# Kernel optimization log

Measured on AMD Instinct MI355X. Metric: run time of the kernel, lower is better.

The kernel has to match this reference:

```python
import jax, jax.numpy as jnp
import numpy as np

STRIDES = (128, 64, 32, 16, 8)
FM_SHAPES = ((6, 10), (12, 20), (24, 40), (48, 80), (96, 160))
RATIOS = np.array([1.0, 2.0, 3.0])
BASE_SIZE = 4
POS_THR, NEG_THR, IGNORE = 0.5, 0.4, -1.0
ALPHA, GAMMA, SIGMA = 0.25, 2.0, 3.0


def _cell_anchors(stride):
    # classic generate_anchors: base 4x4 anchor, 3 aspect ratios, scale=stride
    w = h = float(BASE_SIZE)
    ctr = (BASE_SIZE - 1) / 2.0
    size = w * h
    ws = np.round(np.sqrt(size / RATIOS))
    hs = np.round(ws * RATIOS)
    a = np.stack([ctr - 0.5 * (ws - 1), ctr - 0.5 * (hs - 1),
                  ctr + 0.5 * (ws - 1), ctr + 0.5 * (hs - 1)], 1)
    aw = a[:, 2] - a[:, 0] + 1
    ah = a[:, 3] - a[:, 1] + 1
    cx = a[:, 0] + 0.5 * (aw - 1)
    cy = a[:, 1] + 0.5 * (ah - 1)
    sw = aw * stride
    sh = ah * stride
    return np.stack([cx - 0.5 * (sw - 1), cy - 0.5 * (sh - 1),
                     cx + 0.5 * (sw - 1), cy + 0.5 * (sh - 1)], 1)


def _all_anchors():
    outs = []
    for (h, w), s in zip(FM_SHAPES, STRIDES):
        cell = _cell_anchors(s)  # [3,4]
        sx = np.tile((np.arange(w) * s)[None, :], (h, 1)).reshape(-1)
        sy = np.tile((np.arange(h) * s)[:, None], (1, w)).reshape(-1)
        shifts = np.stack([sx, sy, sx, sy], 1)  # [h*w,4]
        outs.append((cell[None] + shifts[:, None]).reshape(-1, 4))
    return np.concatenate(outs, 0).astype(np.float32)  # [A,4]


def box_overlap(b, g):
    ab = (b[:, 2] - b[:, 0] + 1) * (b[:, 3] - b[:, 1] + 1)
    ag = (g[:, 2] - g[:, 0] + 1) * (g[:, 3] - g[:, 1] + 1)
    iw = jnp.clip(jnp.minimum(b[:, None, 2], g[None, :, 2]) - jnp.maximum(b[:, None, 0], g[None, :, 0]) + 1, 0)
    ih = jnp.clip(jnp.minimum(b[:, None, 3], g[None, :, 3]) - jnp.maximum(b[:, None, 1], g[None, :, 1]) + 1, 0)
    inter = iw * ih
    return inter / (ab[:, None] + ag[None, :] - inter)


def bbox_transform_inv(anc, dlt):
    w = anc[..., 2] - anc[..., 0] + 1
    h = anc[..., 3] - anc[..., 1] + 1
    cx = anc[..., 0] + 0.5 * (w - 1)
    cy = anc[..., 1] + 0.5 * (h - 1)
    mx = jnp.log(jnp.asarray(1000.0 / 16, dlt.dtype))
    pw = jnp.exp(jnp.minimum(dlt[..., 2], mx)) * w
    ph = jnp.exp(jnp.minimum(dlt[..., 3], mx)) * h
    pcx = dlt[..., 0] * w + cx
    pcy = dlt[..., 1] * h + cy
    return jnp.stack([pcx - 0.5 * (pw - 1), pcy - 0.5 * (ph - 1),
                      pcx + 0.5 * (pw - 1), pcy + 0.5 * (ph - 1)], -1)


def bbox_transform(anc, gt):
    aw = anc[..., 2] - anc[..., 0] + 1
    ah = anc[..., 3] - anc[..., 1] + 1
    acx = anc[..., 0] + 0.5 * (aw - 1)
    acy = anc[..., 1] + 0.5 * (ah - 1)
    gw = gt[..., 2] - gt[..., 0] + 1
    gh = gt[..., 3] - gt[..., 1] + 1
    gcx = gt[..., 0] + 0.5 * (gw - 1)
    gcy = gt[..., 1] + 0.5 * (gh - 1)
    return jnp.stack([(gcx - acx) / aw, (gcy - acy) / ah,
                      jnp.log(gw / aw), jnp.log(gh / ah)], -1)


def conv3x3(x, w, b):
    y = jax.lax.conv_general_dilated(x, w, (1, 1), 'SAME',
                                     dimension_numbers=('NCHW', 'OIHW', 'NCHW'))
    return y + b[None, :, None, None]


def _head(feat, cls_w, cls_b, box_w, box_b, score_w, score_b,
          bpred_w, bpred_b, iou_w, iou_b, num_w, num_b):
    n = feat.shape[0]
    c = feat
    for i in range(4):
        c = jax.nn.relu(conv3x3(c, cls_w[i], cls_b[i]))
    cls_prob = jax.nn.sigmoid(conv3x3(c, score_w, score_b))
    num_prob = conv3x3(c, num_w, num_b)
    r = feat
    for i in range(4):
        r = jax.nn.relu(conv3x3(r, box_w[i], box_b[i]))
    offsets = conv3x3(r, bpred_w, bpred_b)
    iou_prob = conv3x3(r, iou_w, iou_b)
    rs = lambda t, ch: t.transpose(0, 2, 3, 1).reshape(n, -1, ch)
    return rs(cls_prob, 2), rs(num_prob, 2), rs(offsets, 8), rs(iou_prob, 2)


def _forward(feats, gt_boxes, im_info, cls_w, cls_b, box_w, box_b,
             score_w, score_b, bpred_w, bpred_b, iou_w, iou_b, num_w, num_b):
    outs = [_head(f, cls_w, cls_b, box_w, box_b, score_w, score_b,
                  bpred_w, bpred_b, iou_w, iou_b, num_w, num_b) for f in feats]
    cls_prob = jnp.concatenate([o[0] for o in outs], 1)  # [n,A,2]
    num_prob = jnp.concatenate([o[1] for o in outs], 1)  # [n,A,2]
    offsets = jnp.concatenate([o[2] for o in outs], 1)   # [n,A,8]
    iou_prob = jnp.concatenate([o[3] for o in outs], 1)  # [n,A,2]
    anchors = jnp.asarray(_all_anchors())                # [A,4]
    A = anchors.shape[0]
    n = cls_prob.shape[0]
    G = gt_boxes.shape[1]
    counts = im_info[:, 5]
    gidx = jnp.arange(G, dtype=jnp.float32)

    def anchor_target_one(gt, cnt):
        valid = (gidx < cnt) & (gt[:, 4] != IGNORE)
        ov = jnp.where(valid[None, :], box_overlap(anchors, gt[:, :4]), -1.0)
        top2, idx = jax.lax.top_k(ov, 2)  # [A,2]
        labels = jnp.where(top2 >= POS_THR, 1.0,
                           jnp.where(top2 < NEG_THR, 0.0, -1.0))
        tgt = bbox_transform(anchors[:, None, :], gt[idx, :4])  # [A,2,4]
        return labels, tgt.reshape(-1, 4)

    rpn_labels, target_boxes = jax.vmap(anchor_target_one)(gt_boxes, counts)
    rpn_labels = jax.lax.stop_gradient(rpn_labels)        # [n,A,2]
    target_boxes = jax.lax.stop_gradient(target_boxes)    # [n,2A,4]
    anchors2 = jnp.repeat(anchors, 2, axis=0)             # [2A,4] interleaved

    def iou_target_one(gt, cnt, off):
        dt = bbox_transform_inv(anchors2, off.reshape(-1, 4))  # [2A,4]
        keep = ((gidx < cnt) & (gt[:, 4] != IGNORE)).astype(dt.dtype)
        ov = box_overlap(dt, gt[:, :4]) * keep[None, :]        # [2A,G]
        ov = ov.reshape(A, 2, G)
        a, b = ov[:, 0], ov[:, 1]
        i1 = jnp.argmax(a, 1)
        av = jnp.take_along_axis(a, i1[:, None], 1)
        b = b.at[jnp.arange(A), i1].set(0.0)
        bv = jnp.max(b, 1, keepdims=True)
        return jnp.concatenate([av, bv], 1)                    # [A,2]

    ious_target = jax.lax.stop_gradient(
        jax.vmap(iou_target_one)(gt_boxes, counts, offsets))

    a, b = rpn_labels[..., 0], rpn_labels[..., 1]
    ignores = b - (a == 0).astype(b.dtype) * (b != 0).astype(b.dtype)
    labels = jnp.stack([a, ignores], 2).reshape(n, -1)     # [n,2A]

    # focal (sigmoid_cross_entropy_retina)
    p = cls_prob.reshape(n, -1, 1)                          # [n,2A,1]
    mask = (labels != IGNORE).astype(p.dtype)
    onehot = ((labels * mask) == 1).astype(p.dtype)[..., None]
    pos = (1 - p) ** GAMMA * onehot * jnp.log(p)
    neg = p ** GAMMA * (1 - onehot) * jnp.log(1 - p)
    npos = jnp.maximum((labels > 0).astype(p.dtype).sum(), 1.0)
    cls_loss = (-(ALPHA * pos + (1 - ALPHA) * neg).sum(-1) * mask).sum() / npos

    # smooth_l1_loss_retina (sigma=3)
    off4 = offsets.reshape(n, -1, 4)                        # [n,2A,4]
    diff = off4 - target_boxes
    ad = jnp.abs(diff)
    s2 = SIGMA * SIGMA
    sl1 = jnp.where(ad < 1.0 / s2, 0.5 * s2 * diff * diff, ad - 0.5 / s2)
    posm = (labels > 0).astype(off4.dtype)
    bbox_loss = (sl1.sum(-1) * posm).sum() / jnp.maximum(posm.sum(), 1.0)

    # iou_l1_loss
    lab2 = labels.reshape(n, -1, 2)                         # [n,A,2]
    ioumask = (lab2 > 0).astype(iou_prob.dtype)
    iou_loss = (jnp.abs(iou_prob.reshape(n, -1, 2) - ious_target) * ioumask).sum() \
        / jnp.maximum(ioumask.sum(), 1.0)

    # softmax_loss over num-per-anchor predictions
    nlabels = (lab2 > 0).sum(2).reshape(-1) - 1             # [n*A] in {-1,0,1}
    score = num_prob.reshape(-1, 2)
    logp = jax.nn.log_softmax(score, -1)
    nm = (nlabels != -1)
    vl = jnp.where(nm, nlabels, 0)
    nmf = nm.astype(score.dtype)
    num_loss = (-(jnp.take_along_axis(logp, vl[:, None], 1)[:, 0]) * nmf).sum() \
        / jnp.maximum(nmf.sum(), 1.0)

    return jnp.stack([cls_loss, 2.0 * bbox_loss, 2.0 * iou_loss, num_loss])


def setup_inputs() -> dict:
    key = jax.random.key(0)
    ks = jax.random.split(key, 24)
    n, G = 2, 32
    inp = {}
    for i, (h, w) in enumerate(FM_SHAPES):
        inp[f"feat_p{7 - i}"] = jax.random.normal(ks[i], (n, 256, h, w), jnp.float32) * 0.5
    x1 = jax.random.uniform(ks[5], (n, G), minval=0.0, maxval=900.0)
    y1 = jax.random.uniform(ks[6], (n, G), minval=0.0, maxval=500.0)
    bw = jax.random.uniform(ks[7], (n, G), minval=32.0, maxval=300.0)
    bh = jax.random.uniform(ks[8], (n, G), minval=32.0, maxval=300.0)
    inp["gt_boxes"] = jnp.stack([x1, y1, x1 + bw, y1 + bh, jnp.ones((n, G))], -1).astype(jnp.float32)
    inp["im_info"] = jnp.tile(jnp.array([[768., 1280., 1., 768., 1280., 24.]], jnp.float32), (n, 1))
    std = 0.01
    inp["cls_w"] = jax.random.normal(ks[9], (4, 256, 256, 3, 3), jnp.float32) * std
    inp["cls_b"] = jnp.zeros((4, 256), jnp.float32)
    inp["box_w"] = jax.random.normal(ks[10], (4, 256, 256, 3, 3), jnp.float32) * std
    inp["box_b"] = jnp.zeros((4, 256), jnp.float32)
    prior_bias = -float(np.log((1 - 0.01) / 0.01))
    inp["score_w"] = jax.random.normal(ks[11], (6, 256, 3, 3), jnp.float32) * std
    inp["score_b"] = jnp.full((6,), prior_bias, jnp.float32)
    inp["bpred_w"] = jax.random.normal(ks[12], (24, 256, 3, 3), jnp.float32) * std
    inp["bpred_b"] = jnp.zeros((24,), jnp.float32)
    inp["iou_w"] = jax.random.normal(ks[13], (6, 256, 3, 3), jnp.float32) * std
    inp["iou_b"] = jnp.zeros((6,), jnp.float32)
    inp["num_w"] = jax.random.normal(ks[14], (6, 256, 3, 3), jnp.float32) * std
    inp["num_b"] = jnp.zeros((6,), jnp.float32)
    return inp


def reference(feat_p7, feat_p6, feat_p5, feat_p4, feat_p3, gt_boxes, im_info,
              cls_w, cls_b, box_w, box_b, score_w, score_b, bpred_w, bpred_b,
              iou_w, iou_b, num_w, num_b):
    feats = [feat_p7, feat_p6, feat_p5, feat_p4, feat_p3]
    return _forward(feats, gt_boxes, im_info, cls_w, cls_b, box_w, box_b,
                    score_w, score_b, bpred_w, bpred_b, iou_w, iou_b, num_w, num_b)
```

## Files before the change

kernel.cpp:

```cpp
#include <hip/hip_runtime.h>
#include <math.h>

#define A_TOTAL 61380
#define NGT 32
#define PTOT 21472

typedef _Float16 f16;
typedef f16 f16x8 __attribute__((ext_vector_type(8)));
typedef float f32x4 __attribute__((ext_vector_type(4)));

__device__ __constant__ int LV_H[5]    = {6, 12, 24, 48, 96};
__device__ __constant__ int LV_W[5]    = {10, 20, 40, 80, 160};
__device__ __constant__ int LV_PB[5]   = {0, 96, 404, 1496, 5596};
__device__ __constant__ int LV_TX[5]   = {1, 2, 3, 5, 10};

typedef __attribute__((address_space(1))) const void* gptr_t;
typedef __attribute__((address_space(3))) void* lptr_t;
__device__ __forceinline__ void cp16_g2l(const void* g, void* l) {
  __builtin_amdgcn_global_load_lds((gptr_t)g, (lptr_t)l, 16, 0, 0);
}

__device__ __forceinline__ void get_tile8(int t, int& lv, int& y0, int& x0)
{
  int local;
  if (t >= 44)      { lv = 4; local = t - 44; }
  else if (t >= 14) { lv = 3; local = t - 14; }
  else if (t >= 5)  { lv = 2; local = t - 5; }
  else if (t >= 1)  { lv = 1; local = t - 1; }
  else              { lv = 0; local = 0; }
  int tX = LV_TX[lv];
  y0 = (local / tX) * 8;
  x0 = (local % tX) * 16;
}

__device__ __forceinline__ void get_tile16(int t, int& lv, int& y0, int& x0)
{
  int local;
  if (t >= 24)      { lv = 4; local = t - 24; }
  else if (t >= 9)  { lv = 3; local = t - 9; }
  else if (t >= 3)  { lv = 2; local = t - 3; }
  else if (t >= 1)  { lv = 1; local = t - 1; }
  else              { lv = 0; local = 0; }
  int tX = LV_TX[lv];
  y0 = (local / tX) * 16;
  x0 = (local % tX) * 16;
}

__device__ __forceinline__ int padded_off(int p)
{
  if (p >= 5100)      { int po = p - 5100; int y = po / 160, x = po - y * 160; return 5596 + (y + 1) * 162 + x + 1; }
  else if (p >= 1260) { int po = p - 1260; int y = po / 80,  x = po - y * 80;  return 1496 + (y + 1) * 82  + x + 1; }
  else if (p >= 300)  { int po = p - 300;  int y = po / 40,  x = po - y * 40;  return 404  + (y + 1) * 42  + x + 1; }
  else if (p >= 60)   { int po = p - 60;   int y = po / 20,  x = po - y * 20;  return 96   + (y + 1) * 22  + x + 1; }
  else                { int y = p / 10, x = p - y * 10;                         return (y + 1) * 12 + x + 1; }
}

__global__ __launch_bounds__(64) void zero_borders(f16* __restrict__ act)
{
  int e = blockIdx.x, b = blockIdx.y, z = blockIdx.z;
  int lv, e0;
  if (e >= 496)      { lv = 4; e0 = e - 496; }
  else if (e >= 236) { lv = 3; e0 = e - 236; }
  else if (e >= 104) { lv = 2; e0 = e - 104; }
  else if (e >= 36)  { lv = 1; e0 = e - 36; }
  else               { lv = 0; e0 = e; }
  int Hp = LV_H[lv] + 2, Wp = LV_W[lv] + 2;
  int y, x;
  if (e0 < Wp)          { y = 0;      x = e0; }
  else if (e0 < 2 * Wp) { y = Hp - 1; x = e0 - Wp; }
  else { int e2 = e0 - 2 * Wp; y = 1 + (e2 >> 1); x = (e2 & 1) ? (Wp - 1) : 0; }
  f16* dst = act + ((size_t)z * 2 * PTOT + (size_t)b * PTOT + LV_PB[lv] + y * Wp + x) * 256
           + threadIdx.x * 4;
  *(uint2*)dst = (uint2){0u, 0u};
}

__global__ __launch_bounds__(256) void feats_to_nhwc(
    const float* __restrict__ f0, const float* __restrict__ f1,
    const float* __restrict__ f2, const float* __restrict__ f3,
    const float* __restrict__ f4, f16* __restrict__ act)
{
  const int b = blockIdx.z;
  const int c0 = blockIdx.y * 32;
  const int p0 = blockIdx.x * 32;
  const int tx = threadIdx.x & 31, ty = threadIdx.x >> 5;
  __shared__ float tl[32][33];

  int p = p0 + tx;
  const float* src = f0; int po = 0;
  if (p >= 5100)      { src = f4; po = p - 5100; }
  else if (p >= 1260) { src = f3; po = p - 1260; }
  else if (p >= 300)  { src = f2; po = p - 300;  }
  else if (p >= 60)   { src = f1; po = p - 60;   }
  else                { src = f0; po = p;        }
  int HW = (p >= 5100) ? 15360 : (p >= 1260) ? 3840 : (p >= 300) ? 960 : (p >= 60) ? 240 : 60;

#pragma unroll
  for (int k = 0; k < 4; ++k) {
    int c = c0 + ty + k * 8;
    float v = 0.f;
    if (p < 20460) v = src[((size_t)b * 256 + c) * HW + po];
    tl[ty + k * 8][tx] = v;
  }
  __syncthreads();
#pragma unroll
  for (int k = 0; k < 4; ++k) {
    int pp = p0 + ty + k * 8;
    if (pp < 20460)
      act[((size_t)b * PTOT + padded_off(pp)) * 256 + c0 + tx] = (f16)tl[tx][ty + k * 8];
  }
}

__global__ __launch_bounds__(256) void prep_tower_w3(
    const float* __restrict__ cls_w, const float* __restrict__ box_w,
    f16* __restrict__ wT)
{
  int blk = blockIdx.x;
  int l = blk >> 8, co = blk & 255;
  const float* src = (l < 4 ? cls_w + (size_t)l * 589824
                            : box_w + (size_t)(l - 4) * 589824)
                   + (size_t)co * 2304;
  __shared__ f16 sm[2304];
  int t = threadIdx.x;
#pragma unroll
  for (int j = 0; j < 9; ++j) sm[t + j * 256] = (f16)src[t + j * 256];
  __syncthreads();
#pragma unroll
  for (int it = 0; it < 2; ++it) {
    int c = t + it * 256;
    if (c < 288) {
      int tap = c >> 5, s = c & 31;
      f16x8 v;
#pragma unroll
      for (int e = 0; e < 8; ++e) v[e] = sm[(s * 8 + e) * 9 + tap];
      *(f16x8*)(wT + ((((size_t)l * 9 + tap) * 32 + s) * 256 + co) * 8) = v;
    }
  }
}

__global__ void prep_head_w3(const float* __restrict__ sw, const float* __restrict__ nw,
                             const float* __restrict__ bw, const float* __restrict__ iw,
                             const float* __restrict__ sb, const float* __restrict__ nb2,
                             const float* __restrict__ bb, const float* __restrict__ ib,
                             f16* __restrict__ wH, float* __restrict__ hb)
{
  int idx = blockIdx.x * 256 + threadIdx.x;
  if (idx < 18432) {
    int p = idx / 9216, rem = idx - p * 9216;
    int tap = rem / 1024, rem2 = rem - tap * 1024;
    int s = rem2 >> 5, co = rem2 & 31;
    int C1 = p ? 24 : 6;
    const float* w1 = p ? bw : sw;
    const float* w2 = p ? iw : nw;
    f16x8 v;
#pragma unroll
    for (int e = 0; e < 8; ++e) {
      int ci = s * 8 + e;
      float x = 0.f;
      if (co < C1)          x = w1[((size_t)co * 256 + ci) * 9 + tap];
      else if (co < C1 + 6) x = w2[((size_t)(co - C1) * 256 + ci) * 9 + tap];
      v[e] = (f16)x;
    }
    *(f16x8*)(wH + (size_t)idx * 8) = v;
  }
  if (idx < 64) {
    int pp = idx >> 5, jj = idx & 31;
    int C1b = pp ? 24 : 6;
    const float* b1 = pp ? bb : sb;
    const float* b2 = pp ? ib : nb2;
    float bv = 0.f;
    if (jj < C1b)          bv = b1[jj];
    else if (jj < C1b + 6) bv = b2[jj - C1b];
    hb[idx] = bv;
  }
}

__global__ __launch_bounds__(256, 2) void conv_mfma_tower4(
    const f16* __restrict__ in_cls, f16* __restrict__ out_cls,
    const f16* __restrict__ in_box, f16* __restrict__ out_box,
    const f16* __restrict__ wT, const float* __restrict__ cls_b,
    const float* __restrict__ box_b, int layer)
{
  int lv, y0, x0;
  get_tile8(blockIdx.x, lv, y0, x0);
  const int H = LV_H[lv], W = LV_W[lv], Wp = W + 2, pbase = LV_PB[lv];
  const int b = blockIdx.y;
  const int z = blockIdx.z, tw = z >> 1, cog = z & 1;
  const f16* in  = tw ? in_box : in_cls;
  f16*       out = tw ? out_box : out_cls;
  const f16* wB = wT + (size_t)(tw * 4 + layer) * 2304 * 256;
  const float* bias = (tw ? box_b : cls_b) + layer * 256;

  const int tid = threadIdx.x;
  const int lane = tid & 63, wid = tid >> 6;
  const int m = lane & 15, q = lane >> 4;
  const int mrow = (wid & 1) * 4;
  const int ncol = (wid >> 1) * 64;

  __shared__ __align__(16) f16 Bs[4096 * 8];

  f32x4 acc[4][4];
#pragma unroll
  for (int i = 0; i < 4; ++i)
#pragma unroll
    for (int j = 0; j < 4; ++j) acc[i][j] = (f32x4){0.f, 0.f, 0.f, 0.f};

  const f16* inb = in + (size_t)(b * PTOT + pbase) * 256;
  const f16* pA = inb + ((size_t)(y0 + mrow) * Wp + x0 + m) * 256 + q * 8;

  for (int cb = 0; cb < 8; ++cb) {
    __syncthreads();
#pragma unroll
    for (int it = 0; it < 16; ++it) {
      int u = tid + it * 256;
      int tap = u >> 9, r = u & 511;
      int s = r >> 7, c = r & 127;
      cp16_g2l(wB + (((size_t)(tap * 32 + cb * 4 + s)) * 256 + cog * 128 + c) * 8,
               Bs + (size_t)u * 8);
    }
    __syncthreads();
    const f16* pAc = pA + cb * 32;
#pragma unroll
    for (int tap = 0; tap < 9; ++tap) {
      const int ky = tap / 3, kx = tap - ky * 3;
      f16x8 af[4], bf[4];
#pragma unroll
      for (int mb = 0; mb < 4; ++mb)
        af[mb] = *(const f16x8*)(pAc + ((size_t)(mb + ky) * Wp + kx) * 256);
      if (tap < 8) {
#pragma unroll
        for (int nb = 0; nb < 4; ++nb)
          bf[nb] = *(const f16x8*)(Bs + (size_t)(tap * 512 + q * 128 + ncol + nb * 16 + m) * 8);
      } else {
#pragma unroll
        for (int nb = 0; nb < 4; ++nb)
          bf[nb] = *(const f16x8*)(wB + (((size_t)(256 + cb * 4 + q)) * 256 + cog * 128 + ncol + nb * 16 + m) * 8);
      }
#pragma unroll
      for (int mb = 0; mb < 4; ++mb)
#pragma unroll
        for (int nb = 0; nb < 4; ++nb)
          acc[mb][nb] = __builtin_amdgcn_mfma_f32_16x16x32_f16(af[mb], bf[nb], acc[mb][nb], 0, 0, 0);
    }
  }

  f16* outb = out + (size_t)(b * PTOT + pbase) * 256;
#pragma unroll
  for (int mb = 0; mb < 4; ++mb) {
    int y = y0 + mrow + mb;
    if (y >= H) continue;
#pragma unroll
    for (int nb = 0; nb < 4; ++nb) {
      int co = cog * 128 + ncol + nb * 16 + m;
      float bi = bias[co];
#pragma unroll
      for (int r = 0; r < 4; ++r) {
        int x = x0 + q * 4 + r;
        if (x < W) {
          float v = fmaxf(acc[mb][nb][r] + bi, 0.f);
          outb[((size_t)(y + 1) * Wp + x + 1) * 256 + co] = (f16)v;
        }
      }
    }
  }
}

__global__ __launch_bounds__(256) void conv_mfma_head3(
    const f16* __restrict__ in_cls, const f16* __restrict__ in_box,
    const f16* __restrict__ wH, const float* __restrict__ hb,
    float* __restrict__ cls_prob, float* __restrict__ num_prob,
    float* __restrict__ offsets, float* __restrict__ iou_prob)
{
  int lv, y0, x0;
  get_tile16(blockIdx.x, lv, y0, x0);
  const int H = LV_H[lv], W = LV_W[lv], Wp = W + 2, pbase = LV_PB[lv];
  const int b = blockIdx.y, z = blockIdx.z;
  const f16* in = z ? in_box : in_cls;
  const f16* wB = wH + (size_t)z * 2304 * 32;
  const float* hbz = hb + z * 32;
  float* o1 = z ? offsets : cls_prob;
  float* o2 = z ? iou_prob : num_prob;
  const int C1 = z ? 24 : 6, P1 = z ? 8 : 2, SIG = z ? 0 : 1;

  const int tid = threadIdx.x;
  const int lane = tid & 63, wid = tid >> 6;
  const int m = lane & 15, q = lane >> 4;

  f32x4 acc[4][2];
#pragma unroll
  for (int i = 0; i < 4; ++i) { acc[i][0] = (f32x4){0,0,0,0}; acc[i][1] = (f32x4){0,0,0,0}; }

  const f16* inb = in + (size_t)(b * PTOT + pbase) * 256;
  const f16* pA = inb + ((size_t)(y0 + wid * 4) * Wp + x0 + m) * 256 + q * 8;
  const f16* pB = wB + ((size_t)q * 32 + m) * 8;

  for (int cb = 0; cb < 8; ++cb) {
    const f16* pAc = pA + cb * 32;
    const f16* pBc = pB + (size_t)cb * 4 * 32 * 8;
#pragma unroll
    for (int tap = 0; tap < 9; ++tap) {
      const int ky = tap / 3, kx = tap - ky * 3;
      f16x8 af[4], bf[2];
#pragma unroll
      for (int mb = 0; mb < 4; ++mb)
        af[mb] = *(const f16x8*)(pAc + ((size_t)(mb + ky) * Wp + kx) * 256);
#pragma unroll
      for (int nb = 0; nb < 2; ++nb)
        bf[nb] = *(const f16x8*)(pBc + (size_t)tap * 8192 + nb * 128);
#pragma unroll
      for (int mb = 0; mb < 4; ++mb)
#pragma unroll
        for (int nb = 0; nb < 2; ++nb)
          acc[mb][nb] = __builtin_amdgcn_mfma_f32_16x16x32_f16(af[mb], bf[nb], acc[mb][nb], 0, 0, 0);
    }
  }

  const int robase = (lv == 0 ? 0 : lv == 1 ? 60 : lv == 2 ? 300 : lv == 3 ? 1260 : 5100) * 3;
#pragma unroll
  for (int mb = 0; mb < 4; ++mb) {
    int y = y0 + wid * 4 + mb;
    if (y >= H) continue;
#pragma unroll
    for (int nb = 0; nb < 2; ++nb) {
      int j = nb * 16 + m;
      if (j >= C1 + 6) continue;
      float bi = hbz[j];
#pragma unroll
      for (int r = 0; r < 4; ++r) {
        int x = x0 + q * 4 + r;
        if (x < W) {
          float v = acc[mb][nb][r] + bi;
          int row0 = robase + (y * W + x) * 3;
          if (j < C1) {
            if (SIG) v = 1.f / (1.f + expf(-v));
            int jd = j / P1;
            o1[((size_t)b * A_TOTAL + row0 + jd) * P1 + (j - jd * P1)] = v;
          } else {
            int jj = j - C1;
            o2[((size_t)b * A_TOTAL + row0 + (jj >> 1)) * 2 + (jj & 1)] = v;
          }
        }
      }
    }
  }
}

__global__ void gen_anchors(float* __restrict__ anchors, float* __restrict__ accum)
{
  int i = blockIdx.x * 256 + threadIdx.x;
  if (blockIdx.x == 0 && threadIdx.x < 8) accum[threadIdx.x] = 0.f;
  if (i >= A_TOTAL) return;
  int off, s, Wl;
  if (i >= 15300)     { off = 15300; s = 8;   Wl = 160; }
  else if (i >= 3780) { off = 3780;  s = 16;  Wl = 80;  }
  else if (i >= 900)  { off = 900;   s = 32;  Wl = 40;  }
  else if (i >= 180)  { off = 180;   s = 64;  Wl = 20;  }
  else                { off = 0;     s = 128; Wl = 10;  }
  int r = i - off;
  int cell = r / 3, a = r - cell * 3;
  int y = cell / Wl, x = cell - y * Wl;
  float wsv = (a == 0) ? 4.f : (a == 1) ? 3.f : 2.f;
  float hsv = (a == 0) ? 4.f : 6.f;
  float sw = wsv * (float)s, sh = hsv * (float)s;
  float cx = (float)(x * s) + 1.5f, cy = (float)(y * s) + 1.5f;
  anchors[i * 4 + 0] = cx - 0.5f * (sw - 1.f);
  anchors[i * 4 + 1] = cy - 0.5f * (sh - 1.f);
  anchors[i * 4 + 2] = cx + 0.5f * (sw - 1.f);
  anchors[i * 4 + 3] = cy + 0.5f * (sh - 1.f);
}

__global__ __launch_bounds__(256) void anchor_target(
    const float* __restrict__ anchors, const float* __restrict__ gt,
    const float* __restrict__ iminfo, float* __restrict__ rpn, float* __restrict__ tgt)
{
  int i = blockIdx.x * 256 + threadIdx.x;
  int b = blockIdx.y;
  if (i >= A_TOTAL) return;
  float cnt = iminfo[b * 6 + 5];
  float ax1 = anchors[i*4+0], ay1 = anchors[i*4+1], ax2 = anchors[i*4+2], ay2 = anchors[i*4+3];
  float aw = ax2 - ax1 + 1.f, ah = ay2 - ay1 + 1.f, ab = aw * ah;
  float v1 = -1e30f, v2 = -1e30f; int i1 = 0, i2 = 0;
  for (int g = 0; g < NGT; ++g) {
    const float* gp = gt + (b * NGT + g) * 5;
    float ov = -1.f;
    if ((float)g < cnt && gp[4] != -1.f) {
      float iw = fmaxf(fminf(ax2, gp[2]) - fmaxf(ax1, gp[0]) + 1.f, 0.f);
      float ih = fmaxf(fminf(ay2, gp[3]) - fmaxf(ay1, gp[1]) + 1.f, 0.f);
      float inter = iw * ih;
      float ag = (gp[2] - gp[0] + 1.f) * (gp[3] - gp[1] + 1.f);
      ov = inter / (ab + ag - inter);
    }
    if (ov > v1)      { v2 = v1; i2 = i1; v1 = ov; i1 = g; }
    else if (ov > v2) { v2 = ov; i2 = g; }
  }
  float l1 = (v1 >= 0.5f) ? 1.f : ((v1 < 0.4f) ? 0.f : -1.f);
  float l2 = (v2 >= 0.5f) ? 1.f : ((v2 < 0.4f) ? 0.f : -1.f);
  rpn[(b * A_TOTAL + i) * 2 + 0] = l1;
  rpn[(b * A_TOTAL + i) * 2 + 1] = l2;
  float acx = ax1 + 0.5f * (aw - 1.f), acy = ay1 + 0.5f * (ah - 1.f);
  int idx2[2] = {i1, i2};
#pragma unroll
  for (int k = 0; k < 2; ++k) {
    const float* gp = gt + (b * NGT + idx2[k]) * 5;
    float gw = gp[2] - gp[0] + 1.f, gh = gp[3] - gp[1] + 1.f;
    float gcx = gp[0] + 0.5f * (gw - 1.f), gcy = gp[1] + 0.5f * (gh - 1.f);
    float* o = tgt + ((size_t)(b * 2 * A_TOTAL) + i * 2 + k) * 4;
    o[0] = (gcx - acx) / aw;  o[1] = (gcy - acy) / ah;
    o[2] = logf(gw / aw);     o[3] = logf(gh / ah);
  }
}

__global__ __launch_bounds__(256) void iou_target(
    const float* __restrict__ anchors, const float* __restrict__ gt,
    const float* __restrict__ iminfo, const float* __restrict__ offsets,
    float* __restrict__ ioust)
{
  int i = blockIdx.x * 256 + threadIdx.x;
  int b = blockIdx.y;
  if (i >= A_TOTAL) return;
  float cnt = iminfo[b * 6 + 5];
  float ax1 = anchors[i*4+0], ay1 = anchors[i*4+1], ax2 = anchors[i*4+2], ay2 = anchors[i*4+3];
  float aw = ax2 - ax1 + 1.f, ah = ay2 - ay1 + 1.f;
  float acx = ax1 + 0.5f * (aw - 1.f), acy = ay1 + 0.5f * (ah - 1.f);
  const float mx = 4.135166556742356f;
  float bx[2][4];
#pragma unroll
  for (int k = 0; k < 2; ++k) {
    const float* d = offsets + ((size_t)(b * A_TOTAL) + i) * 8 + k * 4;
    float pw = expf(fminf(d[2], mx)) * aw;
    float ph = expf(fminf(d[3], mx)) * ah;
    float pcx = d[0] * aw + acx, pcy = d[1] * ah + acy;
    bx[k][0] = pcx - 0.5f * (pw - 1.f); bx[k][1] = pcy - 0.5f * (ph - 1.f);
    bx[k][2] = pcx + 0.5f * (pw - 1.f); bx[k][3] = pcy + 0.5f * (ph - 1.f);
  }
  float area0 = (bx[0][2]-bx[0][0]+1.f) * (bx[0][3]-bx[0][1]+1.f);
  float area1 = (bx[1][2]-bx[1][0]+1.f) * (bx[1][3]-bx[1][1]+1.f);
  float av = -1e30f; int i1 = 0;
  for (int g = 0; g < NGT; ++g) {
    const float* gp = gt + (b * NGT + g) * 5;
    float keep = ((float)g < cnt && gp[4] != -1.f) ? 1.f : 0.f;
    float ag = (gp[2] - gp[0] + 1.f) * (gp[3] - gp[1] + 1.f);
    float iw = fmaxf(fminf(bx[0][2], gp[2]) - fmaxf(bx[0][0], gp[0]) + 1.f, 0.f);
    float ih = fmaxf(fminf(bx[0][3], gp[3]) - fmaxf(bx[0][1], gp[1]) + 1.f, 0.f);
    float inter = iw * ih;
    float ov = inter / (area0 + ag - inter) * keep;
    if (ov > av) { av = ov; i1 = g; }
  }
  float bv = -1e30f;
  for (int g = 0; g < NGT; ++g) {
    float val = 0.f;
    if (g != i1) {
      const float* gp = gt + (b * NGT + g) * 5;
      float keep = ((float)g < cnt && gp[4] != -1.f) ? 1.f : 0.f;
      float ag = (gp[2] - gp[0] + 1.f) * (gp[3] - gp[1] + 1.f);
      float iw = fmaxf(fminf(bx[1][2], gp[2]) - fmaxf(bx[1][0], gp[0]) + 1.f, 0.f);
      float ih = fmaxf(fminf(bx[1][3], gp[3]) - fmaxf(bx[1][1], gp[1]) + 1.f, 0.f);
      float inter = iw * ih;
      val = inter / (area1 + ag - inter) * keep;
    }
    bv = fmaxf(bv, val);
  }
  ioust[(b * A_TOTAL + i) * 2 + 0] = av;
  ioust[(b * A_TOTAL + i) * 2 + 1] = bv;
}

__global__ __launch_bounds__(256) void loss_reduce(
    const float* __restrict__ cls_prob, const float* __restrict__ num_prob,
    const float* __restrict__ offsets,  const float* __restrict__ iou_prob,
    const float* __restrict__ rpn,      const float* __restrict__ tgt,
    const float* __restrict__ ioust,    float* __restrict__ accum)
{
  int i = blockIdx.x * 256 + threadIdx.x;
  int b = blockIdx.y;
  float cls_s = 0.f, npos = 0.f, bb_s = 0.f, iou_s = 0.f, num_s = 0.f, num_c = 0.f;
  float la = 0.f, ign = 0.f;
  if (i < A_TOTAL) {
    int base = b * A_TOTAL + i;
    la = rpn[base * 2 + 0];
    float lb = rpn[base * 2 + 1];
    ign = lb - ((la == 0.f && lb != 0.f) ? 1.f : 0.f);
    float lab2[2] = {la, ign};
#pragma unroll
    for (int j = 0; j < 2; ++j) {
      float l = lab2[j];
      float mask = (l != -1.f) ? 1.f : 0.f;
      bool oh = (l * mask) == 1.f;
      float p = cls_prob[base * 2 + j];
      float term = oh ? (0.25f * (1.f - p) * (1.f - p) * logf(p))
                      : (0.75f * p * p * logf(1.f - p));
      cls_s += -term * mask;
      if (l > 0.f) {
        npos += 1.f;
#pragma unroll
        for (int c = 0; c < 4; ++c) {
          float d = offsets[(size_t)base * 8 + j * 4 + c]
                  - tgt[((size_t)(b * 2 * A_TOTAL) + i * 2 + j) * 4 + c];
          float ad = fabsf(d);
          bb_s += (ad < 1.f / 9.f) ? (4.5f * d * d) : (ad - 0.5f / 9.f);
        }
        iou_s += fabsf(iou_prob[base * 2 + j] - ioust[base * 2 + j]);
      }
    }
    int nl = ((la > 0.f) ? 1 : 0) + ((ign > 0.f) ? 1 : 0) - 1;
    if (nl != -1) {
      float s0 = num_prob[base * 2], s1 = num_prob[base * 2 + 1];
      float mm = fmaxf(s0, s1);
      float lse = mm + logf(expf(s0 - mm) + expf(s1 - mm));
      num_s += lse - ((nl == 0) ? s0 : s1);
      num_c += 1.f;
    }
  }
  __shared__ float red[6][4];
  float vals[6] = {cls_s, npos, bb_s, iou_s, num_s, num_c};
  int lane = threadIdx.x & 63, wid = threadIdx.x >> 6;
#pragma unroll
  for (int qq = 0; qq < 6; ++qq) {
    float v = vals[qq];
#pragma unroll
    for (int o = 32; o > 0; o >>= 1) v += __shfl_down(v, o);
    if (lane == 0) red[qq][wid] = v;
  }
  __syncthreads();
  if (threadIdx.x < 6) {
    float s = red[threadIdx.x][0] + red[threadIdx.x][1] + red[threadIdx.x][2] + red[threadIdx.x][3];
    atomicAdd(&accum[threadIdx.x], s);
  }
}

__global__ void finalize_loss(const float* __restrict__ acc, float* __restrict__ out)
{
  float npos = fmaxf(acc[1], 1.f);
  out[0] = acc[0] / npos;
  out[1] = 2.f * acc[2] / npos;
  out[2] = 2.f * acc[3] / npos;
  out[3] = acc[4] / fmaxf(acc[5], 1.f);
}

extern "C" void kernel_launch(void* const* d_in, const int* in_sizes, int n_in,
                              void* d_out, int out_size, void* d_ws, size_t ws_size,
                              hipStream_t stream)
{
  (void)in_sizes; (void)n_in; (void)out_size; (void)ws_size;
  const float* feat[5];
  for (int i = 0; i < 5; ++i) feat[i] = (const float*)d_in[i];
  const float* gt      = (const float*)d_in[5];
  const float* iminfo  = (const float*)d_in[6];
  const float* cls_w   = (const float*)d_in[7];
  const float* cls_b   = (const float*)d_in[8];
  const float* box_w   = (const float*)d_in[9];
  const float* box_b   = (const float*)d_in[10];
  const float* score_w = (const float*)d_in[11];
  const float* score_b = (const float*)d_in[12];
  const float* bpred_w = (const float*)d_in[13];
  const float* bpred_b = (const float*)d_in[14];
  const float* iou_w   = (const float*)d_in[15];
  const float* iou_b   = (const float*)d_in[16];
  const float* num_w   = (const float*)d_in[17];
  const float* num_b   = (const float*)d_in[18];

  const size_t ACT2 = (size_t)2 * PTOT * 256;
  f16* actF = (f16*)d_ws;
  f16* actA = actF + ACT2;
  f16* actB = actA + ACT2;
  f16* actC = actB + ACT2;
  f16* wT   = actC + ACT2;
  f16* wH   = wT + (size_t)8 * 2304 * 256;
  float* hb = (float*)(wH + (size_t)2 * 2304 * 32);

  float* cls_prob = (float*)actA;
  float* num_prob = cls_prob + 2 * A_TOTAL * 2;
  float* offsets  = num_prob + 2 * A_TOTAL * 2;
  float* iou_prob = offsets + 2 * A_TOTAL * 8;
  float* anchors  = iou_prob + 2 * A_TOTAL * 2;
  float* rpn      = anchors + A_TOTAL * 4;
  float* tgt      = rpn + 2 * A_TOTAL * 2;
  float* ioust    = tgt + 2 * 2 * A_TOTAL * 4;
  float* accum    = ioust + 2 * A_TOTAL * 2;

  prep_tower_w3<<<dim3(2048), 256, 0, stream>>>(cls_w, box_w, wT);
  prep_head_w3<<<dim3(72), 256, 0, stream>>>(
      score_w, num_w, bpred_w, iou_w, score_b, num_b, bpred_b, iou_b, wH, hb);
  zero_borders<<<dim3(1012, 2, 4), 64, 0, stream>>>(actF);
  feats_to_nhwc<<<dim3(640, 8, 2), 256, 0, stream>>>(
      feat[0], feat[1], feat[2], feat[3], feat[4], actF);

  dim3 tg(164, 2, 4);
  conv_mfma_tower4<<<tg, 256, 0, stream>>>(actF, actA, actF, actC, wT, cls_b, box_b, 0);
  conv_mfma_tower4<<<tg, 256, 0, stream>>>(actA, actB, actC, actF, wT, cls_b, box_b, 1);
  conv_mfma_tower4<<<tg, 256, 0, stream>>>(actB, actA, actF, actC, wT, cls_b, box_b, 2);
  conv_mfma_tower4<<<tg, 256, 0, stream>>>(actA, actB, actC, actF, wT, cls_b, box_b, 3);

  conv_mfma_head3<<<dim3(84, 2, 2), 256, 0, stream>>>(
      actB, actF, wH, hb, cls_prob, num_prob, offsets, iou_prob);

  dim3 agrid((A_TOTAL + 255) / 256, 2);
  gen_anchors<<<dim3((A_TOTAL + 255) / 256), 256, 0, stream>>>(anchors, accum);
  anchor_target<<<agrid, 256, 0, stream>>>(anchors, gt, iminfo, rpn, tgt);
  iou_target<<<agrid, 256, 0, stream>>>(anchors, gt, iminfo, offsets, ioust);
  loss_reduce<<<agrid, 256, 0, stream>>>(cls_prob, num_prob, offsets, iou_prob,
                                         rpn, tgt, ioust, accum);
  finalize_loss<<<1, 1, 0, stream>>>(accum, (float*)d_out);
}
```

Baseline: 902.2 us.

## Stage input halo tile in LDS and reuse rows across kernel taps

The tower conv kernel now copies the 10x18-pixel input halo for each 32-channel block into shared memory, where it used to read activations straight from global memory once per tap. Rows are loaded once per kx and reused across the three ky taps. The weight staging buffer shrinks to six taps, with the last-row taps read from global memory. This is meant to cut redundant global activation reads, at the cost of fewer weights staged in LDS and more global weight loads.

```diff
diff --git a/kernel.cpp b/kernel.cpp
--- a/kernel.cpp
+++ b/kernel.cpp
@@ -174,7 +174,7 @@
   }
 }
 
-__global__ __launch_bounds__(256, 2) void conv_mfma_tower4(
+__global__ __launch_bounds__(256, 2) void conv_mfma_tower5(
     const f16* __restrict__ in_cls, f16* __restrict__ out_cls,
     const f16* __restrict__ in_box, f16* __restrict__ out_box,
     const f16* __restrict__ wT, const float* __restrict__ cls_b,
@@ -196,7 +196,8 @@
   const int mrow = (wid & 1) * 4;
   const int ncol = (wid >> 1) * 64;
 
-  __shared__ __align__(16) f16 Bs[4096 * 8];
+  __shared__ __align__(16) f16 Al[720 * 8];
+  __shared__ __align__(16) f16 Bl[3072 * 8];
 
   f32x4 acc[4][4];
 #pragma unroll
@@ -205,41 +206,54 @@
     for (int j = 0; j < 4; ++j) acc[i][j] = (f32x4){0.f, 0.f, 0.f, 0.f};
 
   const f16* inb = in + (size_t)(b * PTOT + pbase) * 256;
-  const f16* pA = inb + ((size_t)(y0 + mrow) * Wp + x0 + m) * 256 + q * 8;
 
   for (int cb = 0; cb < 8; ++cb) {
     __syncthreads();
 #pragma unroll
-    for (int it = 0; it < 16; ++it) {
+    for (int it = 0; it < 3; ++it) {
       int u = tid + it * 256;
-      int tap = u >> 9, r = u & 511;
-      int s = r >> 7, c = r & 127;
-      cp16_g2l(wB + (((size_t)(tap * 32 + cb * 4 + s)) * 256 + cog * 128 + c) * 8,
-               Bs + (size_t)u * 8);
+      if (u < 720) {
+        int r = u / 72, rem = u - r * 72;
+        int s = rem / 18, px = rem - s * 18;
+        cp16_g2l(inb + ((size_t)(y0 + r) * Wp + x0 + px) * 256 + cb * 32 + s * 8,
+                 Al + (size_t)u * 8);
+      }
+    }
+#pragma unroll
+    for (int it = 0; it < 12; ++it) {
+      int u = tid + it * 256;
+      int tapS = u >> 7, col = u & 127;
+      int tap = tapS >> 2, s = tapS & 3;
+      cp16_g2l(wB + (((size_t)(tap * 32 + cb * 4 + s)) * 256 + cog * 128 + col) * 8,
+               Bl + (size_t)u * 8);
     }
     __syncthreads();
-    const f16* pAc = pA + cb * 32;
-#pragma unroll
-    for (int tap = 0; tap < 9; ++tap) {
-      const int ky = tap / 3, kx = tap - ky * 3;
-      f16x8 af[4], bf[4];
-#pragma unroll
-      for (int mb = 0; mb < 4; ++mb)
-        af[mb] = *(const f16x8*)(pAc + ((size_t)(mb + ky) * Wp + kx) * 256);
-      if (tap < 8) {
-#pragma unroll
-        for (int nb = 0; nb < 4; ++nb)
-          bf[nb] = *(const f16x8*)(Bs + (size_t)(tap * 512 + q * 128 + ncol + nb * 16 + m) * 8);
-      } else {
-#pragma unroll
-        for (int nb = 0; nb < 4; ++nb)
-          bf[nb] = *(const f16x8*)(wB + (((size_t)(256 + cb * 4 + q)) * 256 + cog * 128 + ncol + nb * 16 + m) * 8);
+
+#pragma unroll
+    for (int kx = 0; kx < 3; ++kx) {
+      f16x8 rowv[6];
+#pragma unroll
+      for (int rr = 0; rr < 6; ++rr)
+        rowv[rr] = *(const f16x8*)(Al + (size_t)(((mrow + rr) * 4 + q) * 18 + m + kx) * 8);
+#pragma unroll
+      for (int ky = 0; ky < 3; ++ky) {
+        const int tap = ky * 3 + kx;
+        f16x8 bf[4];
+        if (ky < 2) {
+#pragma unroll
+          for (int nb = 0; nb < 4; ++nb)
+            bf[nb] = *(const f16x8*)(Bl + (size_t)((tap * 4 + q) * 128 + ncol + nb * 16 + m) * 8);
+        } else {
+#pragma unroll
+          for (int nb = 0; nb < 4; ++nb)
+            bf[nb] = *(const f16x8*)(wB + (((size_t)(tap * 32 + cb * 4 + q)) * 256 + cog * 128 + ncol + nb * 16 + m) * 8);
+        }
+#pragma unroll
+        for (int mb = 0; mb < 4; ++mb)
+#pragma unroll
+          for (int nb = 0; nb < 4; ++nb)
+            acc[mb][nb] = __builtin_amdgcn_mfma_f32_16x16x32_f16(rowv[mb + ky], bf[nb], acc[mb][nb], 0, 0, 0);
       }
-#pragma unroll
-      for (int mb = 0; mb < 4; ++mb)
-#pragma unroll
-        for (int nb = 0; nb < 4; ++nb)
-          acc[mb][nb] = __builtin_amdgcn_mfma_f32_16x16x32_f16(af[mb], bf[nb], acc[mb][nb], 0, 0, 0);
     }
   }
 
@@ -584,10 +598,10 @@
       feat[0], feat[1], feat[2], feat[3], feat[4], actF);
 
   dim3 tg(164, 2, 4);
-  conv_mfma_tower4<<<tg, 256, 0, stream>>>(actF, actA, actF, actC, wT, cls_b, box_b, 0);
-  conv_mfma_tower4<<<tg, 256, 0, stream>>>(actA, actB, actC, actF, wT, cls_b, box_b, 1);
-  conv_mfma_tower4<<<tg, 256, 0, stream>>>(actB, actA, actF, actC, wT, cls_b, box_b, 2);
-  conv_mfma_tower4<<<tg, 256, 0, stream>>>(actA, actB, actC, actF, wT, cls_b, box_b, 3);
+  conv_mfma_tower5<<<tg, 256, 0, stream>>>(actF, actA, actF, actC, wT, cls_b, box_b, 0);
+  conv_mfma_tower5<<<tg, 256, 0, stream>>>(actA, actB, actC, actF, wT, cls_b, box_b, 1);
+  conv_mfma_tower5<<<tg, 256, 0, stream>>>(actB, actA, actF, actC, wT, cls_b, box_b, 2);
+  conv_mfma_tower5<<<tg, 256, 0, stream>>>(actA, actB, actC, actF, wT, cls_b, box_b, 3);
 
   conv_mfma_head3<<<dim3(84, 2, 2), 256, 0, stream>>>(
       actB, actF, wH, hb, cls_prob, num_prob, offsets, iou_prob);
```

New measurement: 733.1 us. 1.23x faster.
